# Optimization experiments

Hardware: AMD Instinct MI355X
Metric: run time of the kernel (lower is better)

The kernel has to match this reference:

```python
import jax, jax.numpy as jnp
import numpy as np

BINS = 10  # module init arg


def setup_inputs() -> dict:
    key = jax.random.key(0)
    k1, k2 = jax.random.split(key)
    pred = jax.random.normal(k1, (16384, 4096), dtype=jnp.float32)
    target = jax.random.bernoulli(k2, 0.5, (16384, 4096)).astype(jnp.float32)
    return {"pred": pred, "target": target}


def reference(pred, target):
    bins = BINS
    # gradient-norm proxy; sigmoid(pred) is detached in the original
    g = jnp.abs(jax.lax.stop_gradient(jax.nn.sigmoid(pred)) - target)
    tot = jnp.float32(g.size)
    # edges[i] = i/bins with edges[-1] += 1e-6, so bin index = floor(g*bins)
    # clipped to [0, bins-1] (g == 1.0 lands in the last bin).
    idx = jnp.clip(jnp.floor(g * bins).astype(jnp.int32), 0, bins - 1)
    counts = jnp.zeros((bins,), jnp.float32).at[idx.reshape(-1)].add(1.0)
    n = jnp.sum(counts > 0).astype(jnp.float32)  # number of non-empty bins
    per_bin_w = jnp.where(counts > 0, tot / jnp.maximum(counts, 1.0), 0.0)
    weights = per_bin_w[idx] / jnp.maximum(n, 1.0)
    weights = jax.lax.stop_gradient(weights)  # weights carry no grad in torch
    # numerically stable BCE-with-logits, per element
    x, t = pred, target
    bce = jnp.maximum(x, 0.0) - x * t + jnp.log1p(jnp.exp(-jnp.abs(x)))
    return jnp.sum(weights * bce) / tot
```

## Files before the change

kernel.cpp:

```cpp
#include <hip/hip_runtime.h>

#define NBINS 10
#define BLOCK 256
#define GRID  1024
#define NWAVE (BLOCK / 64)

static_assert((long long)GRID * BLOCK * 16 == 0x400000, "quad stride literal must match");


__global__ void ghm_init(double* gU, unsigned* gC) {
    int t = threadIdx.x;
    if (t < NBINS) { gU[t] = 0.0; gC[t] = 0u; }
}

#define THRA(TS, AJ)                                                          \
    "v_cmp_le_f32 vcc, " TS ", v40\n\t"                                       \
    "v_cndmask_b32 v45, 0, v44, vcc\n\t"                                      \
    "v_add_u32 " AJ ", " AJ ", v45\n\t"

#define ELEM_ASM(PX, TX)                                                      \
    "v_fma_f32 v40, " TX ", -2.0, 1.0\n\t"              \
    "v_mul_f32 v40, " PX ", v40\n\t"                                  \
    "v_mul_f32 v41, %[nl2e], abs(v40)\n\t"               \
    "v_exp_f32 v42, v41\n\t"                                    \
    "v_max_f32 v43, 0, v40\n\t"                           \
    "v_add_f32 v41, 1.0, v42\n\t"                               \
    "v_log_f32 v41, v41\n\t"                                \
    "v_cmp_le_f32 vcc, %[tau0], v40\n\t"      \
    "v_fma_f32 v43, %[ln2], v41, v43\n\t"                            \
    "v_fma_f32 v44, %[kq], v43, 0.5\n\t"                    \
    "v_cvt_u32_f32 v44, v44\n\t"                                     \
    "v_add_u32 v44, 0x1000000, v44\n\t"              \
    "v_add_u32 %[u0], %[u0], v44\n\t"                              \
    "v_cndmask_b32 v45, 0, v44, vcc\n\t"                                      \
    "v_add_u32 %[a0], %[a0], v45\n\t"                                         \
    THRA("%[tau1]", "%[a1]")                                                  \
    THRA("%[tau2]", "%[a2]")                                                  \
    THRA("%[tau3]", "%[a3]")                                                  \
    THRA("0",       "%[a4]")                                                  \
    THRA("%[tau5]", "%[a5]")                                                  \
    THRA("%[tau6]", "%[a6]")                                                  \
    THRA("%[tau7]", "%[a7]")                                                  \
    THRA("%[tau8]", "%[a8]")

#define QUADC(P0,P1,P2,P3,T0,T1,T2,T3)                                        \
    ELEM_ASM(P0,T0) ELEM_ASM(P1,T1) ELEM_ASM(P2,T2) ELEM_ASM(P3,T3)

#define QUAD_A QUADC("v48","v49","v50","v51","v52","v53","v54","v55")
#define QUAD_B QUADC("v56","v57","v58","v59","v60","v61","v62","v63")
#define QUAD_C QUADC("v64","v65","v66","v67","v68","v69","v70","v71")
#define QUAD_D QUADC("v72","v73","v74","v75","v76","v77","v78","v79")

#define ISSUE_S(SP, ST)                                                       \
    "global_load_dwordx4 " SP ", %[off], %[pb] sc0\n\t"                       \
    "global_load_dwordx4 " ST ", %[off], %[tb] sc0\n\t"                       \
    "v_add_u32 %[off], 0x400000, %[off]\n\t"

#define ISSUE_A ISSUE_S("v[48:51]", "v[52:55]")
#define ISSUE_B ISSUE_S("v[56:59]", "v[60:63]")
#define ISSUE_C ISSUE_S("v[64:67]", "v[68:71]")
#define ISSUE_D ISSUE_S("v[72:75]", "v[76:79]")

__global__ __launch_bounds__(BLOCK, 4) void ghm_main(const float4* __restrict__ pred,
                                                     const float4* __restrict__ targ,
                                                     int n4,
                                                     double* __restrict__ gU,
                                                     unsigned* __restrict__ gC) {
    const float TAUH[9] = {-2.19722458f, -1.38629436f, -0.84729786f, -0.40546511f, 0.0f,
                            0.40546511f,  0.84729786f,  1.38629436f,  2.19722458f};

    const int stride = GRID * BLOCK;
    const int i = blockIdx.x * BLOCK + threadIdx.x;
    const int nq = (n4 % stride == 0) ? (n4 / stride) : -1;

    unsigned Sfx[NBINS];
    unsigned Cnt[NBINS];
#pragma unroll
    for (int j = 0; j < NBINS; ++j) { Sfx[j] = 0u; Cnt[j] = 0u; }

    if (nq > 0 && (nq % 32) == 0) {
        const int nhalf = nq / 32;
        unsigned off = (unsigned)i * 16u;
        for (int h = 0; h < nhalf; ++h) {
            unsigned u0 = 0u, a0 = 0u, a1 = 0u, a2 = 0u, a3 = 0u, a4 = 0u,
                     a5 = 0u, a6 = 0u, a7 = 0u, a8 = 0u;
            int cnt = 7;

            asm volatile(
                ISSUE_A ISSUE_B ISSUE_C ISSUE_D
                "Lmain_%=:\n\t"
                "s_waitcnt vmcnt(6)\n\t" QUAD_A ISSUE_A
                "s_waitcnt vmcnt(6)\n\t" QUAD_B ISSUE_B
                "s_waitcnt vmcnt(6)\n\t" QUAD_C ISSUE_C
                "s_waitcnt vmcnt(6)\n\t" QUAD_D ISSUE_D
                "s_sub_u32 %[cnt], %[cnt], 1\n\t"
                "s_cmp_lg_u32 %[cnt], 0\n\t"
                "s_cbranch_scc1 Lmain_%=\n\t"
                "s_waitcnt vmcnt(6)\n\t" QUAD_A
                "s_waitcnt vmcnt(4)\n\t" QUAD_B
                "s_waitcnt vmcnt(2)\n\t" QUAD_C
                "s_waitcnt vmcnt(0)\n\t" QUAD_D
                : [u0]"+v"(u0), [a0]"+v"(a0), [a1]"+v"(a1), [a2]"+v"(a2),
                  [a3]"+v"(a3), [a4]"+v"(a4), [a5]"+v"(a5), [a6]"+v"(a6),
                  [a7]"+v"(a7), [a8]"+v"(a8), [off]"+v"(off), [cnt]"+s"(cnt)
                : [pb]"s"(pred), [tb]"s"(targ),
                  [nl2e]"s"(-1.44269504f), [ln2]"s"(0.69314718f), [kq]"s"(4096.0f),
                  [tau0]"s"(TAUH[0]), [tau1]"s"(TAUH[1]), [tau2]"s"(TAUH[2]),
                  [tau3]"s"(TAUH[3]), [tau5]"s"(TAUH[5]), [tau6]"s"(TAUH[6]),
                  [tau7]"s"(TAUH[7]), [tau8]"s"(TAUH[8])
                : "vcc", "scc", "memory",
                  "v40","v41","v42","v43","v44","v45",
                  "v48","v49","v50","v51","v52","v53","v54","v55",
                  "v56","v57","v58","v59","v60","v61","v62","v63",
                  "v64","v65","v66","v67","v68","v69","v70","v71",
                  "v72","v73","v74","v75","v76","v77","v78","v79");

            Sfx[0] += u0 - (128u << 24);  Cnt[0] += 128u;
            unsigned aa[9] = {a0,a1,a2,a3,a4,a5,a6,a7,a8};
#pragma unroll
            for (int j = 0; j < 9; ++j) {
                Sfx[1 + j] += aa[j] & 0xFFFFFFu;
                Cnt[1 + j] += aa[j] >> 24;
            }
        }
    } else {
        for (int k = i; k < n4; k += stride) {
            float4 p = pred[k];
            float4 t = targ[k];
            float px[4] = {p.x, p.y, p.z, p.w};
            float tx[4] = {t.x, t.y, t.z, t.w};
            for (int e = 0; e < 4; ++e) {
                float xp = px[e] * fmaf(-2.0f, tx[e], 1.0f);
                float e2 = __builtin_amdgcn_exp2f(fabsf(xp) * -1.44269504f);
                float bce = fmaf(0.69314718f, __builtin_amdgcn_logf(1.0f + e2),
                                 fmaxf(xp, 0.0f));
                unsigned bfx = (unsigned)(fmaf(4096.0f, bce, 0.5f));
                Sfx[0] += bfx; Cnt[0] += 1u;
#pragma unroll
                for (int j = 0; j < 9; ++j) {
                    bool pg = (xp >= TAUH[j]);
                    Sfx[1 + j] += pg ? bfx : 0u;
                    Cnt[1 + j] += pg ? 1u : 0u;
                }
            }
        }
    }

#pragma unroll
    for (int j = 0; j < NBINS; ++j) {
#pragma unroll
        for (int m = 1; m < 64; m <<= 1) {
            Sfx[j] += (unsigned)__shfl_xor((int)Sfx[j], m, 64);
            Cnt[j] += (unsigned)__shfl_xor((int)Cnt[j], m, 64);
        }
    }

    __shared__ unsigned sS[NWAVE][NBINS];
    __shared__ unsigned sC[NWAVE][NBINS];
    const int wid  = threadIdx.x >> 6;
    const int lane = threadIdx.x & 63;
    if (lane == 0) {
#pragma unroll
        for (int j = 0; j < NBINS; ++j) { sS[wid][j] = Sfx[j]; sC[wid][j] = Cnt[j]; }
    }
    __syncthreads();

    if (threadIdx.x < NBINS) {
        unsigned s = 0u, c = 0u;
#pragma unroll
        for (int w = 0; w < NWAVE; ++w) { s += sS[w][threadIdx.x]; c += sC[w][threadIdx.x]; }
        atomicAdd(&gU[threadIdx.x], (double)s);
        if (threadIdx.x > 0) atomicAdd(&gC[threadIdx.x], c);
    }
}

__global__ void ghm_finalize(const double* __restrict__ gU,
                             const unsigned* __restrict__ gC,
                             float* __restrict__ out, unsigned ntot) {
    if (threadIdx.x == 0 && blockIdx.x == 0) {
        double acc = 0.0;
        int n = 0;
        for (int b = 0; b < NBINS; ++b) {
            double   hiU = (b < 9) ? gU[b + 1] : 0.0;
            unsigned hiC = (b < 9) ? gC[b + 1] : 0u;
            double   S = (gU[b] - hiU) * (1.0 / 4096.0);
            unsigned c = ((b == 0) ? ntot : gC[b]) - hiC;
            if (c > 0u) {
                ++n;
                acc += S / (double)c;
            }
        }
        if (n < 1) n = 1;
        out[0] = (float)(acc / (double)n);
    }
}

extern "C" void kernel_launch(void* const* d_in, const int* in_sizes, int n_in,
                              void* d_out, int out_size, void* d_ws, size_t ws_size,
                              hipStream_t stream) {
    const float4* pred = (const float4*)d_in[0];
    const float4* targ = (const float4*)d_in[1];
    double*   gU = (double*)d_ws;
    unsigned* gC = (unsigned*)((char*)d_ws + NBINS * sizeof(double));
    float* out = (float*)d_out;

    int n4 = in_sizes[0] / 4;
    unsigned ntot = (unsigned)in_sizes[0];

    ghm_init<<<1, 64, 0, stream>>>(gU, gC);
    ghm_main<<<GRID, BLOCK, 0, stream>>>(pred, targ, n4, gU, gC);
    ghm_finalize<<<1, 64, 0, stream>>>(gU, gC, out, ntot);
}
```

Baseline: 115.9 us.

## Give each block a contiguous region with staggered start offsets

Replaces the grid-stride access pattern, where every block touches the whole array in lockstep, with per-block contiguous regions: each block walks its own slice in 4 KB steps per phase. Each block also starts at a rotated offset within its region (a multiple of 8 steps) and wraps around, to spread concurrent DRAM traffic across channels. Runs are split into chunks of up to 32 steps so the packed 24-bit accumulators and the count correction stay valid for shorter runs. This aims to improve DRAM page locality and channel balance, at the cost of more complex loop control and a per-chunk element correction.

```diff
diff --git a/kernel.cpp b/kernel.cpp
--- a/kernel.cpp
+++ b/kernel.cpp
@@ -5,7 +5,7 @@
 #define GRID  1024
 #define NWAVE (BLOCK / 64)
 
-static_assert((long long)GRID * BLOCK * 16 == 0x400000, "quad stride literal must match");
+static_assert(BLOCK * 16 == 0x1000, "per-phase step literal must equal BLOCK*16");
 
 
 __global__ void ghm_init(double* gU, unsigned* gC) {
@@ -54,7 +54,7 @@
 #define ISSUE_S(SP, ST)                                                       \
     "global_load_dwordx4 " SP ", %[off], %[pb] sc0\n\t"                       \
     "global_load_dwordx4 " ST ", %[off], %[tb] sc0\n\t"                       \
-    "v_add_u32 %[off], 0x400000, %[off]\n\t"
+    "v_add_u32 %[off], 0x1000, %[off]\n\t"
 
 #define ISSUE_A ISSUE_S("v[48:51]", "v[52:55]")
 #define ISSUE_B ISSUE_S("v[56:59]", "v[60:63]")
@@ -69,62 +69,74 @@
     const float TAUH[9] = {-2.19722458f, -1.38629436f, -0.84729786f, -0.40546511f, 0.0f,
                             0.40546511f,  0.84729786f,  1.38629436f,  2.19722458f};
 
-    const int stride = GRID * BLOCK;
-    const int i = blockIdx.x * BLOCK + threadIdx.x;
-    const int nq = (n4 % stride == 0) ? (n4 / stride) : -1;
-
     unsigned Sfx[NBINS];
     unsigned Cnt[NBINS];
 #pragma unroll
     for (int j = 0; j < NBINS; ++j) { Sfx[j] = 0u; Cnt[j] = 0u; }
 
-    if (nq > 0 && (nq % 32) == 0) {
-        const int nhalf = nq / 32;
-        unsigned off = (unsigned)i * 16u;
-        for (int h = 0; h < nhalf; ++h) {
-            unsigned u0 = 0u, a0 = 0u, a1 = 0u, a2 = 0u, a3 = 0u, a4 = 0u,
-                     a5 = 0u, a6 = 0u, a7 = 0u, a8 = 0u;
-            int cnt = 7;
-
-            asm volatile(
-                ISSUE_A ISSUE_B ISSUE_C ISSUE_D
-                "Lmain_%=:\n\t"
-                "s_waitcnt vmcnt(6)\n\t" QUAD_A ISSUE_A
-                "s_waitcnt vmcnt(6)\n\t" QUAD_B ISSUE_B
-                "s_waitcnt vmcnt(6)\n\t" QUAD_C ISSUE_C
-                "s_waitcnt vmcnt(6)\n\t" QUAD_D ISSUE_D
-                "s_sub_u32 %[cnt], %[cnt], 1\n\t"
-                "s_cmp_lg_u32 %[cnt], 0\n\t"
-                "s_cbranch_scc1 Lmain_%=\n\t"
-                "s_waitcnt vmcnt(6)\n\t" QUAD_A
-                "s_waitcnt vmcnt(4)\n\t" QUAD_B
-                "s_waitcnt vmcnt(2)\n\t" QUAD_C
-                "s_waitcnt vmcnt(0)\n\t" QUAD_D
-                : [u0]"+v"(u0), [a0]"+v"(a0), [a1]"+v"(a1), [a2]"+v"(a2),
-                  [a3]"+v"(a3), [a4]"+v"(a4), [a5]"+v"(a5), [a6]"+v"(a6),
-                  [a7]"+v"(a7), [a8]"+v"(a8), [off]"+v"(off), [cnt]"+s"(cnt)
-                : [pb]"s"(pred), [tb]"s"(targ),
-                  [nl2e]"s"(-1.44269504f), [ln2]"s"(0.69314718f), [kq]"s"(4096.0f),
-                  [tau0]"s"(TAUH[0]), [tau1]"s"(TAUH[1]), [tau2]"s"(TAUH[2]),
-                  [tau3]"s"(TAUH[3]), [tau5]"s"(TAUH[5]), [tau6]"s"(TAUH[6]),
-                  [tau7]"s"(TAUH[7]), [tau8]"s"(TAUH[8])
-                : "vcc", "scc", "memory",
-                  "v40","v41","v42","v43","v44","v45",
-                  "v48","v49","v50","v51","v52","v53","v54","v55",
-                  "v56","v57","v58","v59","v60","v61","v62","v63",
-                  "v64","v65","v66","v67","v68","v69","v70","v71",
-                  "v72","v73","v74","v75","v76","v77","v78","v79");
-
-            Sfx[0] += u0 - (128u << 24);  Cnt[0] += 128u;
-            unsigned aa[9] = {a0,a1,a2,a3,a4,a5,a6,a7,a8};
-#pragma unroll
-            for (int j = 0; j < 9; ++j) {
-                Sfx[1 + j] += aa[j] & 0xFFFFFFu;
-                Cnt[1 + j] += aa[j] >> 24;
+    const int perBlock = n4 / GRID;
+    const int P = perBlock / BLOCK;
+
+    if ((n4 % (GRID * BLOCK)) == 0 && P >= 8 && (P % 8) == 0) {
+        const unsigned regionBase = (unsigned)blockIdx.x * (unsigned)perBlock * 16u;
+        const unsigned tbase = regionBase + (unsigned)threadIdx.x * 16u;
+        const int r = 8 * (int)(blockIdx.x % (unsigned)(P / 8));
+
+        int runs[2] = {P - r, r};
+        int p0 = r;
+        for (int q = 0; q < 2; ++q) {
+            int run = runs[q];
+            if (q == 1) p0 = 0;
+            while (run > 0) {
+                int L = run > 32 ? 32 : run;
+                unsigned off = tbase + (unsigned)p0 * 4096u;
+                int cnt = (L >> 2) - 1;
+                unsigned u0 = 0u, a0 = 0u, a1 = 0u, a2 = 0u, a3 = 0u, a4 = 0u,
+                         a5 = 0u, a6 = 0u, a7 = 0u, a8 = 0u;
+
+                asm volatile(
+                    ISSUE_A ISSUE_B ISSUE_C ISSUE_D
+                    "Lmain_%=:\n\t"
+                    "s_waitcnt vmcnt(6)\n\t" QUAD_A ISSUE_A
+                    "s_waitcnt vmcnt(6)\n\t" QUAD_B ISSUE_B
+                    "s_waitcnt vmcnt(6)\n\t" QUAD_C ISSUE_C
+                    "s_waitcnt vmcnt(6)\n\t" QUAD_D ISSUE_D
+                    "s_sub_u32 %[cnt], %[cnt], 1\n\t"
+                    "s_cmp_lg_u32 %[cnt], 0\n\t"
+                    "s_cbranch_scc1 Lmain_%=\n\t"
+                    "s_waitcnt vmcnt(6)\n\t" QUAD_A
+                    "s_waitcnt vmcnt(4)\n\t" QUAD_B
+                    "s_waitcnt vmcnt(2)\n\t" QUAD_C
+                    "s_waitcnt vmcnt(0)\n\t" QUAD_D
+                    : [u0]"+v"(u0), [a0]"+v"(a0), [a1]"+v"(a1), [a2]"+v"(a2),
+                      [a3]"+v"(a3), [a4]"+v"(a4), [a5]"+v"(a5), [a6]"+v"(a6),
+                      [a7]"+v"(a7), [a8]"+v"(a8), [off]"+v"(off), [cnt]"+s"(cnt)
+                    : [pb]"s"(pred), [tb]"s"(targ),
+                      [nl2e]"s"(-1.44269504f), [ln2]"s"(0.69314718f), [kq]"s"(4096.0f),
+                      [tau0]"s"(TAUH[0]), [tau1]"s"(TAUH[1]), [tau2]"s"(TAUH[2]),
+                      [tau3]"s"(TAUH[3]), [tau5]"s"(TAUH[5]), [tau6]"s"(TAUH[6]),
+                      [tau7]"s"(TAUH[7]), [tau8]"s"(TAUH[8])
+                    : "vcc", "scc", "memory",
+                      "v40","v41","v42","v43","v44","v45",
+                      "v48","v49","v50","v51","v52","v53","v54","v55",
+                      "v56","v57","v58","v59","v60","v61","v62","v63",
+                      "v64","v65","v66","v67","v68","v69","v70","v71",
+                      "v72","v73","v74","v75","v76","v77","v78","v79");
+
+                const unsigned elems = (unsigned)(L * 4);
+                Sfx[0] += u0 - (elems << 24);  Cnt[0] += elems;
+                unsigned aa[9] = {a0,a1,a2,a3,a4,a5,a6,a7,a8};
+#pragma unroll
+                for (int j = 0; j < 9; ++j) {
+                    Sfx[1 + j] += aa[j] & 0xFFFFFFu;
+                    Cnt[1 + j] += aa[j] >> 24;
+                }
+                p0 += L; run -= L;
             }
         }
     } else {
-        for (int k = i; k < n4; k += stride) {
+        const int stride = GRID * BLOCK;
+        for (int k = blockIdx.x * BLOCK + threadIdx.x; k < n4; k += stride) {
             float4 p = pred[k];
             float4 t = targ[k];
             float px[4] = {p.x, p.y, p.z, p.w};
```

Result: faster. 111.6 us (-3.7%).
